# Kernel tuning notes

Measured on AMD Instinct MI355X. Metric: run time of the kernel, lower is better.

## Reference

```python
import jax, jax.numpy as jnp
import numpy as np
import math

B, T, N, E = 16, 12, 2000, 8000
D, GAT_HEADS, NHEAD, FF, L, HORIZON = 64, 4, 4, 128, 2, 3
M = B * N  # batched node count


def setup_inputs() -> dict:
    key = jax.random.key(0)
    ks = jax.random.split(key, 16)

    def nrm(k, shape, s=0.1):
        return jax.random.normal(k, shape, jnp.float32) * s

    return dict(
        x_seq=jax.random.normal(ks[0], (B, T, N), jnp.float32),
        edge_index=jax.random.randint(ks[1], (2, E), 0, N),
        # GATConv 1: in_dim=1 -> 4 heads x 8 = 32
        W1=nrm(ks[2], (1, 32)),
        att_src1=nrm(ks[3], (GAT_HEADS, 8)),
        att_dst1=nrm(ks[4], (GAT_HEADS, 8)),
        b1=jnp.zeros((32,), jnp.float32),
        # GATConv 2: 32 -> 4 heads x 16 = 64
        W2=nrm(ks[5], (32, 64)),
        att_src2=nrm(ks[6], (GAT_HEADS, 16)),
        att_dst2=nrm(ks[7], (GAT_HEADS, 16)),
        b2=jnp.zeros((64,), jnp.float32),
        # TransformerEncoder (post-LN, relu), stacked over L layers
        Wqkv=nrm(ks[8], (L, 3 * D, D)), bqkv=jnp.zeros((L, 3 * D), jnp.float32),
        Wo=nrm(ks[9], (L, D, D)), bo=jnp.zeros((L, D), jnp.float32),
        Wf1=nrm(ks[10], (L, FF, D)), bf1=jnp.zeros((L, FF), jnp.float32),
        Wf2=nrm(ks[11], (L, D, FF)), bf2=jnp.zeros((L, D), jnp.float32),
        g1=jnp.ones((L, D), jnp.float32), be1=jnp.zeros((L, D), jnp.float32),
        g2=jnp.ones((L, D), jnp.float32), be2=jnp.zeros((L, D), jnp.float32),
        # prediction head
        Wh=nrm(ks[12], (HORIZON, D)), bh=jnp.zeros((HORIZON,), jnp.float32),
    )


def _layer_norm(x, g, b, eps=1e-5):
    mu = x.mean(-1, keepdims=True)
    var = ((x - mu) ** 2).mean(-1, keepdims=True)
    return (x - mu) * jax.lax.rsqrt(var + eps) * g + b


def _gat(x, src, dst, W, a_src, a_dst, bias, H, C, num_nodes):
    # PyG GATConv (concat=True, eval mode). x: [M, in] -> [M, H*C]
    h = (x @ W).reshape(-1, H, C)                                  # [M,H,C]
    e = jax.nn.leaky_relu((h * a_src).sum(-1)[src] + (h * a_dst).sum(-1)[dst], 0.2)  # [Etot,H]
    m = jax.ops.segment_max(e, dst, num_segments=num_nodes)
    w = jnp.exp(e - m[dst])
    s = jax.ops.segment_sum(w, dst, num_segments=num_nodes)
    alpha = w / (s[dst] + 1e-16)
    out = jax.ops.segment_sum(h[src] * alpha[:, :, None], dst, num_segments=num_nodes)
    return out.reshape(-1, H * C) + bias


def _forward(x_seq, edge_index, W1, att_src1, att_dst1, b1, W2, att_src2, att_dst2, b2,
             Wqkv, bqkv, Wo, bo, Wf1, bf1, Wf2, bf2, g1, be1, g2, be2, Wh, bh):
    # batch edge index with per-graph node offsets, then add self loops (PyG default)
    offs = (jnp.arange(B) * N)[:, None]
    loops = jnp.arange(M)
    src = jnp.concatenate([(edge_index[0][None] + offs).reshape(-1), loops])
    dst = jnp.concatenate([(edge_index[1][None] + offs).reshape(-1), loops])

    xt = x_seq.transpose(1, 0, 2).reshape(T, M, 1)  # per-timestep node features

    def gnn_step(x):
        h = jax.nn.relu(_gat(x, src, dst, W1, att_src1, att_dst1, b1, GAT_HEADS, 8, M))
        return jax.nn.relu(_gat(h, src, dst, W2, att_src2, att_dst2, b2, GAT_HEADS, 16, M))

    seq = jax.vmap(gnn_step)(xt)  # [T, M, D]

    # sinusoidal positional encoding over time axis
    pos = jnp.arange(T, dtype=jnp.float32)[:, None]
    div = jnp.exp(jnp.arange(0, D, 2, dtype=jnp.float32) * (-math.log(10000.0) / D))
    pe = jnp.zeros((T, D), jnp.float32)
    pe = pe.at[:, 0::2].set(jnp.sin(pos * div)).at[:, 1::2].set(jnp.cos(pos * div))
    seq = seq + pe[:, None, :]

    hd = D // NHEAD
    scale = 1.0 / math.sqrt(hd)
    for i in range(L):  # post-LN transformer encoder layers
        qkv = seq @ Wqkv[i].T + bqkv[i]
        q, k, v = jnp.split(qkv, 3, axis=-1)
        q = q.reshape(T, M, NHEAD, hd)
        k = k.reshape(T, M, NHEAD, hd)
        v = v.reshape(T, M, NHEAD, hd)
        sc = jnp.einsum('tmhd,smhd->mhts', q, k) * scale  # [M,H,T,T]
        attn = jax.nn.softmax(sc, axis=-1)
        o = jnp.einsum('mhts,smhd->tmhd', attn, v).reshape(T, M, D)
        seq = _layer_norm(seq + (o @ Wo[i].T + bo[i]), g1[i], be1[i])
        ff = jax.nn.relu(seq @ Wf1[i].T + bf1[i]) @ Wf2[i].T + bf2[i]
        seq = _layer_norm(seq + ff, g2[i], be2[i])

    final = seq[-1]  # [M, D]
    return (final @ Wh.T + bh).reshape(B, N, HORIZON).transpose(0, 2, 1)  # [B, horizon, N]


def reference(x_seq, edge_index, W1, att_src1, att_dst1, b1, W2, att_src2, att_dst2, b2,
              Wqkv, bqkv, Wo, bo, Wf1, bf1, Wf2, bf2, g1, be1, g2, be2, Wh, bh):
    return _forward(x_seq, edge_index, W1, att_src1, att_dst1, b1, W2, att_src2, att_dst2, b2,
                    Wqkv, bqkv, Wo, bo, Wf1, bf1, Wf2, bf2, g1, be1, g2, be2, Wh, bh)
```

## Files before the change

### kernel.cpp

```cpp
#include <hip/hip_runtime.h>
#include <hip/hip_bf16.h>

#define B_ 16
#define T_ 12
#define N_ 2000
#define E_ 8000
#define M_ 32000
#define ETOT (B_*E_ + M_)
#define D_ 64

typedef __hip_bfloat16 bf16;
typedef unsigned short u16;
typedef __attribute__((ext_vector_type(8))) _Float16 half8;
typedef __attribute__((ext_vector_type(2))) _Float16 h2v;
typedef __attribute__((ext_vector_type(4))) float f32x4;

__device__ __forceinline__ float bfu(u16 u){ return __uint_as_float(((unsigned int)u)<<16); }
__device__ __forceinline__ u16 f2bu(float f){
  unsigned int x = __float_as_uint(f);
  x += 0x7FFFu + ((x >> 16) & 1u);
  return (u16)(x >> 16);
}
__device__ __forceinline__ u16 f2h(float f){
  _Float16 h = (_Float16)f; u16 r; __builtin_memcpy(&r, &h, 2); return r;
}
__device__ __forceinline__ float h2f(u16 u){
  _Float16 h; __builtin_memcpy(&h, &u, 2); return (float)h;
}
__device__ __forceinline__ h2v u2h(unsigned u){ h2v r; __builtin_memcpy(&r,&u,4); return r; }

__device__ __forceinline__ int xcd_swz(int x, int n){
  int q = n>>3, r = n&7;
  int xcd = x&7, idx = x>>3;
  int base = (xcd<r) ? xcd*(q+1) : r*(q+1) + (xcd-r)*q;
  return base + idx;
}

__global__ void k_prep(const float* __restrict__ Wqkv, const float* __restrict__ Wo,
                       const float* __restrict__ Wf1, const float* __restrict__ Wf2,
                       const float* __restrict__ W2g,
                       u16* __restrict__ wqB, u16* __restrict__ woB,
                       u16* __restrict__ w1B, u16* __restrict__ w2B,
                       float* __restrict__ peT, u16* __restrict__ w2gB){
  int i = blockIdx.x*256 + threadIdx.x;
  if(i < 24576){
    int l=i/12288, r=i-l*12288;
    int nt=r>>10, r2=r&1023, c=r2>>9, r3=r2&511, lane=r3>>3, jj=r3&7;
    int m=lane&15, q=lane>>4;
    wqB[i] = f2h(Wqkv[l*12288 + (nt*16+m)*64 + c*32 + q*8 + jj]);
  } else if(i < 32768){
    int k2=i-24576;
    int l=k2>>12, r=k2&4095;
    int nt=r>>10, r2=r&1023, c=r2>>9, r3=r2&511, lane=r3>>3, jj=r3&7;
    int m=lane&15, q=lane>>4;
    woB[k2] = f2h(Wo[l*4096 + (nt*16+m)*64 + c*32 + q*8 + jj]);
  } else if(i < 49152){
    int k2=i-32768;
    int l=k2>>13, r=k2&8191;
    int nt=r>>10, r2=r&1023, c=r2>>9, r3=r2&511, lane=r3>>3, jj=r3&7;
    int m=lane&15, q=lane>>4;
    w1B[k2] = f2h(Wf1[l*8192 + (nt*16+m)*64 + c*32 + q*8 + jj]);
  } else if(i < 65536){
    int k2=i-49152;
    int l=k2>>13, r=k2&8191;
    int nt=r>>11, r2=r&2047, c=r2>>9, r3=r2&511, lane=r3>>3, jj=r3&7;
    int m=lane&15, q=lane>>4;
    w2B[k2] = f2h(Wf2[l*8192 + (nt*16+m)*128 + c*32 + q*8 + jj]);
  } else {
    int i2 = i - 65536;
    if(i2 < 768){
      int t=i2>>6, ch=i2&63;
      float ang = (float)t * __expf(-0.14391156463f * (float)(ch & ~1));
      peT[i2] = (ch&1) ? __cosf(ang) : __sinf(ang);
    } else if(i2 < 768+2048){
      int i3 = i2-768;
      int nt=i3>>9, r=i3&511, lane=r>>3, j=r&7;
      int m=lane&15, q=lane>>4;
      w2gB[i3] = f2h(W2g[(q*8+j)*64 + nt*16 + m]);
    }
  }
}

__global__ void k_hist(const int* __restrict__ ei, int* __restrict__ deg){
  int e = blockIdx.x*256 + threadIdx.x; if(e>=ETOT) return;
  int dst;
  if (e < B_*E_){ int b = e / E_; int k = e - b*E_; dst = ei[E_ + k] + b*N_; }
  else dst = e - B_*E_;
  atomicAdd(&deg[dst], 1);
}

__global__ void k_scan1(const int* __restrict__ deg, int* __restrict__ offs, int* __restrict__ bsums){
  __shared__ int s[256];
  int tid = threadIdx.x; int g = blockIdx.x*256 + tid;
  s[tid] = deg[g]; __syncthreads();
  for(int off=1; off<256; off<<=1){
    int a = (tid>=off) ? s[tid-off] : 0; __syncthreads();
    s[tid] += a; __syncthreads();
  }
  offs[g+1] = s[tid];
  if(tid==255) bsums[blockIdx.x] = s[255];
}

__global__ void k_scan23(int* __restrict__ offs, const int* __restrict__ bsums){
  __shared__ int s[128];
  int tid = threadIdx.x; int g = blockIdx.x*256 + tid;
  if(tid<128) s[tid] = (tid<125) ? bsums[tid] : 0;
  __syncthreads();
  for(int off=1; off<128; off<<=1){
    int a = 0;
    if(tid<128 && tid>=off) a = s[tid-off];
    __syncthreads();
    if(tid<128) s[tid] += a;
    __syncthreads();
  }
  int boff = (blockIdx.x==0) ? 0 : s[blockIdx.x-1];
  offs[g+1] += boff;
  if(g==0) offs[0]=0;
}

__global__ void k_scatter(const int* __restrict__ ei, const int* __restrict__ offs,
                          int* __restrict__ cursor, int* __restrict__ csr){
  int e = blockIdx.x*256 + threadIdx.x; if(e>=ETOT) return;
  int srcl, dst;
  if (e < B_*E_){ int b=e/E_; int k=e-b*E_; srcl=ei[k]; dst=ei[E_+k]+b*N_; }
  else { dst = e - B_*E_; int b=dst/N_; srcl = dst - b*N_; }
  int pos = atomicAdd(&cursor[dst], 1);
  csr[offs[dst]+pos] = srcl;
}

__global__ __launch_bounds__(256) void k_gat12(
  const float* __restrict__ x_seq, const float* __restrict__ W1,
  const float* __restrict__ as1, const float* __restrict__ ad1, const float* __restrict__ b1,
  const float* __restrict__ as2, const float* __restrict__ ad2,
  const int* __restrict__ offs, const int* __restrict__ csr,
  const u16* __restrict__ w2gB,
  u16* __restrict__ h2u, float* __restrict__ asc, float* __restrict__ adc)
{
  int tid = threadIdx.x, w = tid>>6, lane = tid&63;
  int m = lane&15, q = lane>>4;
  int t = blockIdx.y;
  int bx = xcd_swz(blockIdx.x, 500);
  int node = bx*64 + w*16 + m;
  unsigned un=(unsigned)node, b=un/N_, n=un-b*N_;

  const half8* wb = (const half8*)w2gB;
  half8 w2f0 = wb[0*64+lane], w2f1 = wb[1*64+lane],
        w2f2 = wb[2*64+lane], w2f3 = wb[3*64+lane];

  float sS[4], sD[4];
  #pragma unroll
  for(int h=0;h<4;h++){
    float a=0.f, d=0.f;
    #pragma unroll
    for(int c=0;c<8;c++){ float wv=W1[h*8+c]; a+=wv*as1[h*8+c]; d+=wv*ad1[h*8+c]; }
    sS[h]=a; sD[h]=d;
  }

  const float* xsl = x_seq + (size_t)(b*T_+t)*N_;
  float xm = xsl[n];
  int e0=offs[node], e1=offs[node+1];
  float sum[4]={0.f,0.f,0.f,0.f}, ax[4]={0.f,0.f,0.f,0.f};
  for(int e=e0+q; e<e1; e+=4){
    float xv = xsl[csr[e]];
    #pragma unroll
    for(int h=0;h<4;h++){
      float ee = xv*sS[h] + xm*sD[h]; ee = ee>0.f ? ee : 0.2f*ee;
      float wv = __expf(ee); sum[h]+=wv; ax[h]+=wv*xv;
    }
  }
  #pragma unroll
  for(int h=0;h<4;h++){
    sum[h] += __shfl_xor(sum[h],16); sum[h] += __shfl_xor(sum[h],32);
    ax[h]  += __shfl_xor(ax[h],16);  ax[h]  += __shfl_xor(ax[h],32);
  }
  float A = ax[q]/(sum[q]+1e-16f);

  half8 af;
  #pragma unroll
  for(int j=0;j<8;j++){
    float v = A*W1[q*8+j] + b1[q*8+j]; v = v>0.f?v:0.f;
    af[j] = (_Float16)v;
  }
  f32x4 ac0={0.f,0.f,0.f,0.f}, ac1=ac0, ac2=ac0, ac3=ac0;
  ac0 = __builtin_amdgcn_mfma_f32_16x16x32_f16(w2f0, af, ac0,0,0,0);
  ac1 = __builtin_amdgcn_mfma_f32_16x16x32_f16(w2f1, af, ac1,0,0,0);
  ac2 = __builtin_amdgcn_mfma_f32_16x16x32_f16(w2f2, af, ac2,0,0,0);
  ac3 = __builtin_amdgcn_mfma_f32_16x16x32_f16(w2f3, af, ac3,0,0,0);

  size_t nd = (size_t)t*M_ + node;
  u16* row = h2u + nd*64;
  {
    uint2 p;
    p.x = (unsigned)f2bu(ac0[0]) | ((unsigned)f2bu(ac0[1])<<16);
    p.y = (unsigned)f2bu(ac0[2]) | ((unsigned)f2bu(ac0[3])<<16);
    *(uint2*)(row + 0*16 + q*4) = p;
    p.x = (unsigned)f2bu(ac1[0]) | ((unsigned)f2bu(ac1[1])<<16);
    p.y = (unsigned)f2bu(ac1[2]) | ((unsigned)f2bu(ac1[3])<<16);
    *(uint2*)(row + 1*16 + q*4) = p;
    p.x = (unsigned)f2bu(ac2[0]) | ((unsigned)f2bu(ac2[1])<<16);
    p.y = (unsigned)f2bu(ac2[2]) | ((unsigned)f2bu(ac2[3])<<16);
    *(uint2*)(row + 2*16 + q*4) = p;
    p.x = (unsigned)f2bu(ac3[0]) | ((unsigned)f2bu(ac3[1])<<16);
    p.y = (unsigned)f2bu(ac3[2]) | ((unsigned)f2bu(ac3[3])<<16);
    *(uint2*)(row + 3*16 + q*4) = p;
  }

  const float* a2sp = as2 + q*4;
  const float* a2dp = ad2 + q*4;
  float ps[4], pd[4];
  ps[0]=ac0[0]*a2sp[ 0]+ac0[1]*a2sp[ 1]+ac0[2]*a2sp[ 2]+ac0[3]*a2sp[ 3];
  ps[1]=ac1[0]*a2sp[16]+ac1[1]*a2sp[17]+ac1[2]*a2sp[18]+ac1[3]*a2sp[19];
  ps[2]=ac2[0]*a2sp[32]+ac2[1]*a2sp[33]+ac2[2]*a2sp[34]+ac2[3]*a2sp[35];
  ps[3]=ac3[0]*a2sp[48]+ac3[1]*a2sp[49]+ac3[2]*a2sp[50]+ac3[3]*a2sp[51];
  pd[0]=ac0[0]*a2dp[ 0]+ac0[1]*a2dp[ 1]+ac0[2]*a2dp[ 2]+ac0[3]*a2dp[ 3];
  pd[1]=ac1[0]*a2dp[16]+ac1[1]*a2dp[17]+ac1[2]*a2dp[18]+ac1[3]*a2dp[19];
  pd[2]=ac2[0]*a2dp[32]+ac2[1]*a2dp[33]+ac2[2]*a2dp[34]+ac2[3]*a2dp[35];
  pd[3]=ac3[0]*a2dp[48]+ac3[1]*a2dp[49]+ac3[2]*a2dp[50]+ac3[3]*a2dp[51];
  #pragma unroll
  for(int h=0;h<4;h++){
    ps[h] += __shfl_xor(ps[h],16); ps[h] += __shfl_xor(ps[h],32);
    pd[h] += __shfl_xor(pd[h],16); pd[h] += __shfl_xor(pd[h],32);
  }
  float ra = (q&1) ? ((q&2)? ps[3]:ps[1]) : ((q&2)? ps[2]:ps[0]);
  float rd = (q&1) ? ((q&2)? pd[3]:pd[1]) : ((q&2)? pd[2]:pd[0]);
  asc[nd*4+q] = ra;
  adc[nd*4+q] = rd;
}

__global__ __launch_bounds__(256) void k_gat2b(
  const u16* __restrict__ h2u, const float* __restrict__ asc, const float* __restrict__ adc,
  const float* __restrict__ b2, const int* __restrict__ offs, const int* __restrict__ csr,
  const float* __restrict__ peT, u16* __restrict__ seq)
{
  int t = blockIdx.y;
  int id = xcd_swz(blockIdx.x, 1000)*256 + threadIdx.x;
  int m = id>>3, j = (id>>2)&1, h = id&3;
  unsigned um=(unsigned)m, b=um/N_;
  size_t base_s = (size_t)t*M_ + (size_t)b*N_;
  float am = adc[((size_t)t*M_+m)*4+h];
  int e0=offs[m], e1=offs[m+1];
  float sum=0.f;
  float A[16];
  #pragma unroll
  for(int c=0;c<16;c++) A[c]=0.f;
  for(int e=e0+j; e<e1; e+=2){
    size_t s = base_s + (unsigned)csr[e];
    float ee = asc[s*4+h] + am; ee = ee>0.f ? ee : 0.2f*ee;
    float w = __expf(ee); sum += w;
    const uint4* hp = (const uint4*)(h2u + s*64 + h*16);
    uint4 p0 = hp[0], p1 = hp[1];
    A[ 0] += w*bfu((u16)(p0.x)); A[ 1] += w*bfu((u16)(p0.x>>16));
    A[ 2] += w*bfu((u16)(p0.y)); A[ 3] += w*bfu((u16)(p0.y>>16));
    A[ 4] += w*bfu((u16)(p0.z)); A[ 5] += w*bfu((u16)(p0.z>>16));
    A[ 6] += w*bfu((u16)(p0.w)); A[ 7] += w*bfu((u16)(p0.w>>16));
    A[ 8] += w*bfu((u16)(p1.x)); A[ 9] += w*bfu((u16)(p1.x>>16));
    A[10] += w*bfu((u16)(p1.y)); A[11] += w*bfu((u16)(p1.y>>16));
    A[12] += w*bfu((u16)(p1.z)); A[13] += w*bfu((u16)(p1.z>>16));
    A[14] += w*bfu((u16)(p1.w)); A[15] += w*bfu((u16)(p1.w>>16));
  }
  sum += __shfl_xor(sum,4);
  #pragma unroll
  for(int c=0;c<16;c++) A[c] += __shfl_xor(A[c],4);

  float inv = 1.f/(sum + 1e-16f);
  u16 ov[8];
  #pragma unroll
  for(int c=0;c<8;c++){
    int ch = h*16 + j*8 + c;
    float v = A[j*8+c]*inv + b2[ch]; v = v>0.f ? v : 0.f;
    ov[c] = f2h(v + peT[t*64+ch]);
  }
  uint4 o;
  o.x = (unsigned)ov[0] | ((unsigned)ov[1]<<16);
  o.y = (unsigned)ov[2] | ((unsigned)ov[3]<<16);
  o.z = (unsigned)ov[4] | ((unsigned)ov[5]<<16);
  o.w = (unsigned)ov[6] | ((unsigned)ov[7]<<16);
  *(uint4*)(seq + ((size_t)t*M_ + m)*64 + h*16 + j*8) = o;
}

__global__ __launch_bounds__(192) void k_layer2(
  const u16* __restrict__ seq,
  const u16* __restrict__ wqB, const u16* __restrict__ woB,
  const u16* __restrict__ w1B, const u16* __restrict__ w2B,
  const float* __restrict__ bqkv, const float* __restrict__ bo,
  const float* __restrict__ bf1,  const float* __restrict__ bf2,
  const float* __restrict__ g1,   const float* __restrict__ be1,
  const float* __restrict__ g2,   const float* __restrict__ be2,
  const float* __restrict__ Wh,   const float* __restrict__ bh,
  float* __restrict__ out)
{
  __shared__ __align__(16) u16 X[3456];
  __shared__ __align__(16) u16 QKV[10368];
  u16* Hd = QKV + 3456;
  int tid=threadIdx.x, w=tid>>6, lane=tid&63;
  int m=lane&15, q=lane>>4;
  int r = w*16 + m;

  #pragma unroll
  for(int half=0; half<2; half++){
    int rr = half*8 + (lane>>3);
    int row = w*16 + rr;
    int nn = row/12, tt = row-nn*12;
    const uint4* src = (const uint4*)(seq + ((size_t)tt*M_ + (size_t)blockIdx.x*4+nn)*64) + (lane&7);
    *((uint4*)&X[row*72] + (lane&7)) = *src;
  }

  #pragma unroll 1
  for(int l=0; l<2; l++){
    const half8* wqv = (const half8*)(wqB + (size_t)l*12288);
    const half8* wov = (const half8*)(woB + (size_t)l*4096);
    const half8* w1v = (const half8*)(w1B + (size_t)l*8192);
    const half8* w2v = (const half8*)(w2B + (size_t)l*8192);
    const float* bq = bqkv + l*192;
    const float* boL = bo + l*64;
    const float* b1L = bf1 + l*128;
    const float* b2L = bf2 + l*64;
    const float* g1L = g1 + l*64, *be1L = be1 + l*64;
    const float* g2L = g2 + l*64, *be2L = be2 + l*64;

    half8 xa0 = *(const half8*)&X[r*72 + q*8];
    half8 xa1 = *(const half8*)&X[r*72 + 32 + q*8];
    #pragma unroll
    for(int nt=0; nt<12; nt++){
      f32x4 acc={0.f,0.f,0.f,0.f};
      acc = __builtin_amdgcn_mfma_f32_16x16x32_f16(xa0, wqv[(nt*2+0)*64+lane], acc,0,0,0);
      acc = __builtin_amdgcn_mfma_f32_16x16x32_f16(xa1, wqv[(nt*2+1)*64+lane], acc,0,0,0);
      int cg = nt*16+m; float bias = bq[cg];
      int s = nt>>2, lc = cg&63;
      #pragma unroll
      for(int rg=0;rg<4;rg++){
        int row = w*16 + q*4 + rg;
        QKV[s*3456 + row*72 + lc] = f2h(acc[rg]+bias);
      }
    }
    __syncthreads();

    {
      int an = tid/48, rem = tid - an*48;
      int ah = rem/12, at = rem - ah*12;
      u16* qrow = &QKV[(an*12+at)*72 + ah*16];
      uint4 qa = ((const uint4*)qrow)[0], qb = ((const uint4*)qrow)[1];
      float s[12];
      #pragma unroll
      for(int t2=0;t2<12;t2++){
        const uint4* kp = (const uint4*)&QKV[3456 + (an*12+t2)*72 + ah*16];
        uint4 ka=kp[0], kb=kp[1];
        float d=0.f;
        d=__builtin_amdgcn_fdot2(u2h(qa.x),u2h(ka.x),d,false);
        d=__builtin_amdgcn_fdot2(u2h(qa.y),u2h(ka.y),d,false);
        d=__builtin_amdgcn_fdot2(u2h(qa.z),u2h(ka.z),d,false);
        d=__builtin_amdgcn_fdot2(u2h(qa.w),u2h(ka.w),d,false);
        d=__builtin_amdgcn_fdot2(u2h(qb.x),u2h(kb.x),d,false);
        d=__builtin_amdgcn_fdot2(u2h(qb.y),u2h(kb.y),d,false);
        d=__builtin_amdgcn_fdot2(u2h(qb.z),u2h(kb.z),d,false);
        d=__builtin_amdgcn_fdot2(u2h(qb.w),u2h(kb.w),d,false);
        s[t2] = d*0.25f;
      }
      float mx=s[0];
      #pragma unroll
      for(int t2=1;t2<12;t2++) mx=fmaxf(mx,s[t2]);
      float sum=0.f;
      #pragma unroll
      for(int t2=0;t2<12;t2++){ s[t2]=__expf(s[t2]-mx); sum+=s[t2]; }
      float inv=1.f/sum;
      half8 o0, o1;
      #pragma unroll
      for(int i=0;i<8;i++){ o0[i]=(_Float16)0.f; o1[i]=(_Float16)0.f; }
      #pragma unroll
      for(int t2=0;t2<12;t2++){
        const half8* vr = (const half8*)&QKV[6912 + (an*12+t2)*72 + ah*16];
        _Float16 wh = (_Float16)s[t2];
        o0 += vr[0]*wh; o1 += vr[1]*wh;
      }
      _Float16 ih = (_Float16)inv;
      ((half8*)qrow)[0]=o0*ih; ((half8*)qrow)[1]=o1*ih;
    }
    __syncthreads();

    half8 oa0 = *(const half8*)&QKV[r*72 + q*8];
    half8 oa1 = *(const half8*)&QKV[r*72 + 32 + q*8];
    float y[4][4];
    #pragma unroll
    for(int nt=0;nt<4;nt++){
      f32x4 acc={0.f,0.f,0.f,0.f};
      acc = __builtin_amdgcn_mfma_f32_16x16x32_f16(oa0, wov[(nt*2+0)*64+lane], acc,0,0,0);
      acc = __builtin_amdgcn_mfma_f32_16x16x32_f16(oa1, wov[(nt*2+1)*64+lane], acc,0,0,0);
      int col=nt*16+m; float bias=boL[col];
      #pragma unroll
      for(int rg=0;rg<4;rg++)
        y[nt][rg] = acc[rg] + bias + h2f(X[(w*16+q*4+rg)*72 + col]);
    }
    float mu[4], rs[4];
    #pragma unroll
    for(int rg=0;rg<4;rg++){
      float sm=(y[0][rg]+y[1][rg])+(y[2][rg]+y[3][rg]);
      sm+=__shfl_xor(sm,1); sm+=__shfl_xor(sm,2); sm+=__shfl_xor(sm,4); sm+=__shfl_xor(sm,8);
      mu[rg]=sm*(1.f/64.f);
      float d0=y[0][rg]-mu[rg],d1=y[1][rg]-mu[rg],d2=y[2][rg]-mu[rg],d3=y[3][rg]-mu[rg];
      float vv=(d0*d0+d1*d1)+(d2*d2+d3*d3);
      vv+=__shfl_xor(vv,1); vv+=__shfl_xor(vv,2); vv+=__shfl_xor(vv,4); vv+=__shfl_xor(vv,8);
      rs[rg]=rsqrtf(vv*(1.f/64.f)+1e-5f);
    }
    #pragma unroll
    for(int nt=0;nt<4;nt++){
      int col=nt*16+m; float g=g1L[col], be=be1L[col];
      #pragma unroll
      for(int rg=0;rg<4;rg++){
        float v=(y[nt][rg]-mu[rg])*rs[rg]*g+be;
        y[nt][rg]=v;
        QKV[(w*16+q*4+rg)*72 + col]=f2h(v);
      }
    }

    half8 ya0 = *(const half8*)&QKV[r*72 + q*8];
    half8 ya1 = *(const half8*)&QKV[r*72 + 32 + q*8];
    #pragma unroll
    for(int nt=0;nt<8;nt++){
      f32x4 acc={0.f,0.f,0.f,0.f};
      acc = __builtin_amdgcn_mfma_f32_16x16x32_f16(ya0, w1v[(nt*2+0)*64+lane], acc,0,0,0);
      acc = __builtin_amdgcn_mfma_f32_16x16x32_f16(ya1, w1v[(nt*2+1)*64+lane], acc,0,0,0);
      float bias=b1L[nt*16+m];
      #pragma unroll
      for(int rg=0;rg<4;rg++)
        Hd[(w*16+q*4+rg)*136 + nt*16+m] = f2h(fmaxf(acc[rg]+bias, 0.f));
    }

    half8 ha[4];
    #pragma unroll
    for(int c=0;c<4;c++)
      ha[c] = *(const half8*)&Hd[r*136 + c*32 + q*8];
    #pragma unroll
    for(int nt=0;nt<4;nt++){
      f32x4 acc={0.f,0.f,0.f,0.f};
      #pragma unroll
      for(int c=0;c<4;c++)
        acc = __builtin_amdgcn_mfma_f32_16x16x32_f16(ha[c], w2v[(nt*4+c)*64+lane], acc,0,0,0);
      int col=nt*16+m; float bias=b2L[col];
      #pragma unroll
      for(int rg=0;rg<4;rg++)
        y[nt][rg] = acc[rg] + bias + y[nt][rg];
    }
    #pragma unroll
    for(int rg=0;rg<4;rg++){
      float sm=(y[0][rg]+y[1][rg])+(y[2][rg]+y[3][rg]);
      sm+=__shfl_xor(sm,1); sm+=__shfl_xor(sm,2); sm+=__shfl_xor(sm,4); sm+=__shfl_xor(sm,8);
      mu[rg]=sm*(1.f/64.f);
      float d0=y[0][rg]-mu[rg],d1=y[1][rg]-mu[rg],d2=y[2][rg]-mu[rg],d3=y[3][rg]-mu[rg];
      float vv=(d0*d0+d1*d1)+(d2*d2+d3*d3);
      vv+=__shfl_xor(vv,1); vv+=__shfl_xor(vv,2); vv+=__shfl_xor(vv,4); vv+=__shfl_xor(vv,8);
      rs[rg]=rsqrtf(vv*(1.f/64.f)+1e-5f);
    }
    if(l==0){
      #pragma unroll
      for(int nt=0;nt<4;nt++){
        int col=nt*16+m; float g=g2L[col], be=be2L[col];
        #pragma unroll
        for(int rg=0;rg<4;rg++)
          X[(w*16+q*4+rg)*72 + col] = f2h((y[nt][rg]-mu[rg])*rs[rg]*g + be);
      }
      __syncthreads();
    } else {
      int rc = w*16 + q*4 + 3;
      int nn = rc/12;
      if(rc - nn*12 == 11){
        float vfin[4];
        #pragma unroll
        for(int nt=0;nt<4;nt++){
          int col=nt*16+m;
          vfin[nt] = (y[nt][3]-mu[3])*rs[3]*g2L[col] + be2L[col];
        }
        int gm = blockIdx.x*4 + nn;
        unsigned bb=(unsigned)gm/N_, n2=(unsigned)gm-bb*N_;
        #pragma unroll
        for(int h3=0;h3<3;h3++){
          float p = vfin[0]*Wh[h3*64+m]    + vfin[1]*Wh[h3*64+16+m]
                  + vfin[2]*Wh[h3*64+32+m] + vfin[3]*Wh[h3*64+48+m];
          p += __shfl_xor(p,1); p += __shfl_xor(p,2);
          p += __shfl_xor(p,4); p += __shfl_xor(p,8);
          if(m==0) out[(bb*3+h3)*N_+n2] = p + bh[h3];
        }
      }
    }
  }
}

extern "C" void kernel_launch(void* const* d_in, const int* in_sizes, int n_in,
                              void* d_out, int out_size, void* d_ws, size_t ws_size,
                              hipStream_t stream)
{
  const float* x_seq=(const float*)d_in[0];
  const int*   ei   =(const int*)d_in[1];
  const float* W1   =(const float*)d_in[2];
  const float* as1  =(const float*)d_in[3];
  const float* ad1  =(const float*)d_in[4];
  const float* b1   =(const float*)d_in[5];
  const float* W2   =(const float*)d_in[6];
  const float* as2  =(const float*)d_in[7];
  const float* ad2  =(const float*)d_in[8];
  const float* b2   =(const float*)d_in[9];
  const float* Wqkv =(const float*)d_in[10];
  const float* bqkv =(const float*)d_in[11];
  const float* Wo   =(const float*)d_in[12];
  const float* bo   =(const float*)d_in[13];
  const float* Wf1  =(const float*)d_in[14];
  const float* bf1p =(const float*)d_in[15];
  const float* Wf2  =(const float*)d_in[16];
  const float* bf2p =(const float*)d_in[17];
  const float* g1   =(const float*)d_in[18];
  const float* be1  =(const float*)d_in[19];
  const float* g2   =(const float*)d_in[20];
  const float* be2  =(const float*)d_in[21];
  const float* Wh   =(const float*)d_in[22];
  const float* bh   =(const float*)d_in[23];

  u16* seqh   = (u16*)d_ws;
  float* asc  = (float*)(seqh + 24576000);
  float* adc  = asc + 1536000;
  int* deg    = (int*)(adc + 1536000);
  int* cursor = deg + M_;
  int* offs   = cursor + M_;
  int* bsums  = offs + (M_ + 2);
  int* boffs  = bsums + 128;
  int* csr    = boffs + 128;
  u16* h2u    = (u16*)(csr + ETOT);
  u16* wqB    = h2u + (size_t)T_*M_*64;
  u16* woB    = wqB + 24576;
  u16* w1B    = woB + 8192;
  u16* w2B    = w1B + 16384;
  float* peT  = (float*)(w2B + 16384);
  u16* w2gB   = (u16*)(peT + 768);

  k_prep   <<<dim3(268), dim3(256), 0, stream>>>(Wqkv, Wo, Wf1, Wf2, W2,
                                                 wqB, woB, w1B, w2B, peT, w2gB);

  hipMemsetAsync(deg, 0, (size_t)2*M_*sizeof(int), stream);
  k_hist   <<<dim3((ETOT+255)/256), dim3(256), 0, stream>>>(ei, deg);
  k_scan1  <<<dim3(125), dim3(256), 0, stream>>>(deg, offs, bsums);
  k_scan23 <<<dim3(125), dim3(256), 0, stream>>>(offs, bsums);
  k_scatter<<<dim3((ETOT+255)/256), dim3(256), 0, stream>>>(ei, offs, cursor, csr);

  k_gat12<<<dim3(500,T_), dim3(256), 0, stream>>>(x_seq, W1, as1, ad1, b1,
                                                  as2, ad2, offs, csr, w2gB,
                                                  h2u, asc, adc);
  k_gat2b<<<dim3(1000,T_), dim3(256), 0, stream>>>(h2u, asc, adc, b2, offs, csr, peT, seqh);

  k_layer2<<<dim3(8000), dim3(192), 0, stream>>>(seqh,
      wqB, woB, w1B, w2B,
      bqkv, bo, bf1p, bf2p,
      g1, be1, g2, be2,
      Wh, bh, (float*)d_out);
}
```

Before: 355.5 us.

## Build a single per-graph CSR shared across batches instead of batched CSR

Every batch element uses the same edge_index, so the code now builds the CSR adjacency once for N nodes (E+N edges including self loops) rather than for all B*N nodes. The GAT kernels index offsets by local node id and add the batch offset to the neighbour index themselves. The two-pass block scan becomes one single-block 1024-thread scan, which removes a kernel launch and shrinks the histogram, scatter and memset work by a factor of B. The saving is limited to the small graph-preprocessing kernels, and the single-block scan runs serially on one CU.

```diff
diff --git a/kernel.cpp b/kernel.cpp
--- a/kernel.cpp
+++ b/kernel.cpp
@@ -6,7 +6,7 @@
 #define N_ 2000
 #define E_ 8000
 #define M_ 32000
-#define ETOT (B_*E_ + M_)
+#define EG (E_ + N_)
 #define D_ 64
 
 typedef __hip_bfloat16 bf16;
@@ -81,49 +81,36 @@
   }
 }
 
-__global__ void k_hist(const int* __restrict__ ei, int* __restrict__ deg){
-  int e = blockIdx.x*256 + threadIdx.x; if(e>=ETOT) return;
-  int dst;
-  if (e < B_*E_){ int b = e / E_; int k = e - b*E_; dst = ei[E_ + k] + b*N_; }
-  else dst = e - B_*E_;
+__global__ void k_histg(const int* __restrict__ ei, int* __restrict__ deg){
+  int e = blockIdx.x*256 + threadIdx.x; if(e>=EG) return;
+  int dst = (e < E_) ? ei[E_+e] : e - E_;
   atomicAdd(&deg[dst], 1);
 }
 
-__global__ void k_scan1(const int* __restrict__ deg, int* __restrict__ offs, int* __restrict__ bsums){
-  __shared__ int s[256];
-  int tid = threadIdx.x; int g = blockIdx.x*256 + tid;
-  s[tid] = deg[g]; __syncthreads();
-  for(int off=1; off<256; off<<=1){
-    int a = (tid>=off) ? s[tid-off] : 0; __syncthreads();
-    s[tid] += a; __syncthreads();
-  }
-  offs[g+1] = s[tid];
-  if(tid==255) bsums[blockIdx.x] = s[255];
-}
-
-__global__ void k_scan23(int* __restrict__ offs, const int* __restrict__ bsums){
-  __shared__ int s[128];
-  int tid = threadIdx.x; int g = blockIdx.x*256 + tid;
-  if(tid<128) s[tid] = (tid<125) ? bsums[tid] : 0;
+__global__ __launch_bounds__(1024) void k_scang(const int* __restrict__ deg, int* __restrict__ offs){
+  __shared__ int s[2048];
+  int tid = threadIdx.x;
+  s[tid]      = (tid      < N_) ? deg[tid]      : 0;
+  s[tid+1024] = (tid+1024 < N_) ? deg[tid+1024] : 0;
   __syncthreads();
-  for(int off=1; off<128; off<<=1){
-    int a = 0;
-    if(tid<128 && tid>=off) a = s[tid-off];
+  for(int off=1; off<2048; off<<=1){
+    int a0 = (tid>=off)      ? s[tid-off]      : 0;
+    int a1 = (tid+1024>=off) ? s[tid+1024-off] : 0;
     __syncthreads();
-    if(tid<128) s[tid] += a;
+    s[tid] += a0; s[tid+1024] += a1;
     __syncthreads();
   }
-  int boff = (blockIdx.x==0) ? 0 : s[blockIdx.x-1];
-  offs[g+1] += boff;
-  if(g==0) offs[0]=0;
-}
-
-__global__ void k_scatter(const int* __restrict__ ei, const int* __restrict__ offs,
-                          int* __restrict__ cursor, int* __restrict__ csr){
-  int e = blockIdx.x*256 + threadIdx.x; if(e>=ETOT) return;
+  if(tid      < N_) offs[tid+1]      = s[tid];
+  if(tid+1024 < N_) offs[tid+1024+1] = s[tid+1024];
+  if(tid==0) offs[0]=0;
+}
+
+__global__ void k_scatg(const int* __restrict__ ei, const int* __restrict__ offs,
+                        int* __restrict__ cursor, int* __restrict__ csr){
+  int e = blockIdx.x*256 + threadIdx.x; if(e>=EG) return;
   int srcl, dst;
-  if (e < B_*E_){ int b=e/E_; int k=e-b*E_; srcl=ei[k]; dst=ei[E_+k]+b*N_; }
-  else { dst = e - B_*E_; int b=dst/N_; srcl = dst - b*N_; }
+  if(e < E_){ srcl = ei[e]; dst = ei[E_+e]; }
+  else      { srcl = e - E_; dst = e - E_; }
   int pos = atomicAdd(&cursor[dst], 1);
   csr[offs[dst]+pos] = srcl;
 }
@@ -158,7 +145,7 @@
 
   const float* xsl = x_seq + (size_t)(b*T_+t)*N_;
   float xm = xsl[n];
-  int e0=offs[node], e1=offs[node+1];
+  int e0=offs[n], e1=offs[n+1];
   float sum[4]={0.f,0.f,0.f,0.f}, ax[4]={0.f,0.f,0.f,0.f};
   for(int e=e0+q; e<e1; e+=4){
     float xv = xsl[csr[e]];
@@ -235,10 +222,10 @@
   int t = blockIdx.y;
   int id = xcd_swz(blockIdx.x, 1000)*256 + threadIdx.x;
   int m = id>>3, j = (id>>2)&1, h = id&3;
-  unsigned um=(unsigned)m, b=um/N_;
+  unsigned um=(unsigned)m, b=um/N_, nl=um-b*N_;
   size_t base_s = (size_t)t*M_ + (size_t)b*N_;
   float am = adc[((size_t)t*M_+m)*4+h];
-  int e0=offs[m], e1=offs[m+1];
+  int e0=offs[nl], e1=offs[nl+1];
   float sum=0.f;
   float A[16];
   #pragma unroll
@@ -516,28 +503,25 @@
   u16* seqh   = (u16*)d_ws;
   float* asc  = (float*)(seqh + 24576000);
   float* adc  = asc + 1536000;
-  int* deg    = (int*)(adc + 1536000);
-  int* cursor = deg + M_;
-  int* offs   = cursor + M_;
-  int* bsums  = offs + (M_ + 2);
-  int* boffs  = bsums + 128;
-  int* csr    = boffs + 128;
-  u16* h2u    = (u16*)(csr + ETOT);
-  u16* wqB    = h2u + (size_t)T_*M_*64;
+  u16* h2u    = (u16*)(adc + 1536000);
+  u16* wqB    = h2u + 24576000;
   u16* woB    = wqB + 24576;
   u16* w1B    = woB + 8192;
   u16* w2B    = w1B + 16384;
   float* peT  = (float*)(w2B + 16384);
   u16* w2gB   = (u16*)(peT + 768);
+  int* deg    = (int*)(w2gB + 2048);
+  int* cursor = deg + N_;
+  int* offs   = cursor + N_;
+  int* csr    = offs + (N_ + 2);
 
   k_prep   <<<dim3(268), dim3(256), 0, stream>>>(Wqkv, Wo, Wf1, Wf2, W2,
                                                  wqB, woB, w1B, w2B, peT, w2gB);
 
-  hipMemsetAsync(deg, 0, (size_t)2*M_*sizeof(int), stream);
-  k_hist   <<<dim3((ETOT+255)/256), dim3(256), 0, stream>>>(ei, deg);
-  k_scan1  <<<dim3(125), dim3(256), 0, stream>>>(deg, offs, bsums);
-  k_scan23 <<<dim3(125), dim3(256), 0, stream>>>(offs, bsums);
-  k_scatter<<<dim3((ETOT+255)/256), dim3(256), 0, stream>>>(ei, offs, cursor, csr);
+  hipMemsetAsync(deg, 0, (size_t)2*N_*sizeof(int), stream);
+  k_histg <<<dim3((EG+255)/256), dim3(256), 0, stream>>>(ei, deg);
+  k_scang <<<dim3(1), dim3(1024), 0, stream>>>(deg, offs);
+  k_scatg <<<dim3((EG+255)/256), dim3(256), 0, stream>>>(ei, offs, cursor, csr);
 
   k_gat12<<<dim3(500,T_), dim3(256), 0, stream>>>(x_seq, W1, as1, ad1, b1,
                                                   as2, ad2, offs, csr, w2gB,
```

After: 345.6 us. 1.03x faster.
